# Kernel tuning notes

Measured on AMD Instinct MI355X. Metric: run time of the kernel, lower is better.

## Reference

```python
import jax, jax.numpy as jnp
import numpy as np

D = 1024
H = 16
HD = D // H


def quant_linear(x, W, b):
    # global abs-max fake quant, then linear (W is [out, in] like torch)
    scale = jnp.abs(x).max() / 127.0 + 1e-8
    xq = jnp.clip(jnp.round(x / scale), -128.0, 127.0) * scale
    return xq @ W.T + b


def rmsnorm(x, w, eps=1e-6):
    ms = jnp.mean(x * x, axis=-1, keepdims=True)
    return w * (x * jax.lax.rsqrt(ms + eps))


def setup_inputs() -> dict:
    key = jax.random.key(0)
    ks = jax.random.split(key, 20)
    def lin(k, out_f, in_f):
        bound = 1.0 / np.sqrt(in_f)
        kw, kb = jax.random.split(k)
        W = jax.random.uniform(kw, (out_f, in_f), jnp.float32, -bound, bound)
        b = jax.random.uniform(kb, (out_f,), jnp.float32, -bound, bound)
        return W, b
    x = jax.random.normal(ks[0], (4, 2048, D), jnp.float32)
    h_prev = jax.random.normal(ks[1], (4, 2048, D), jnp.float32)
    rec_W, rec_b = lin(ks[2], D, D)
    in_proj_w = jax.random.normal(ks[3], (3 * D, D), jnp.float32) * (1.0 / np.sqrt(D))
    in_proj_b = jnp.zeros((3 * D,), jnp.float32)
    out_w, out_b = lin(ks[4], D, D)
    w1_W, w1_b = lin(ks[5], 4 * D, D)
    w2_W, w2_b = lin(ks[6], 4 * D, D)
    w3_W, w3_b = lin(ks[7], D, 4 * D)
    # depthwise conv1d: torch weight [D, 1, 5]
    cb = 1.0 / np.sqrt(5)
    conv_w = jax.random.uniform(ks[8], (D, 1, 5), jnp.float32, -cb, cb)
    conv_b = jax.random.uniform(ks[9], (D,), jnp.float32, -cb, cb)
    return dict(x=x, h_prev=h_prev,
                norm1_w=jnp.ones((D,), jnp.float32), norm2_w=jnp.ones((D,), jnp.float32),
                decay=jnp.full((D,), -0.2, jnp.float32),
                rec_W=rec_W, rec_b=rec_b,
                in_proj_w=in_proj_w, in_proj_b=in_proj_b, out_w=out_w, out_b=out_b,
                conv_w=conv_w, conv_b=conv_b,
                w1_W=w1_W, w1_b=w1_b, w2_W=w2_W, w2_b=w2_b, w3_W=w3_W, w3_b=w3_b)


def reference(x, h_prev, norm1_w, norm2_w, decay, rec_W, rec_b,
              in_proj_w, in_proj_b, out_w, out_b, conv_w, conv_b,
              w1_W, w1_b, w2_W, w2_b, w3_W, w3_b):
    B, S, _ = x.shape
    nx = rmsnorm(x, norm1_w)
    # decay-gated recurrence (single step)
    h_rec = jnp.tanh(quant_linear(nx, rec_W, rec_b) + jnp.exp(decay) * h_prev)
    # multi-head self-attention (torch MultiheadAttention, batch_first)
    qkv = nx @ in_proj_w.T + in_proj_b  # [B,S,3D]
    q, k, v = jnp.split(qkv, 3, axis=-1)
    q = q.reshape(B, S, H, HD)
    k = k.reshape(B, S, H, HD)
    v = v.reshape(B, S, H, HD)
    scores = jnp.einsum('bqhd,bkhd->bhqk', q, k) / np.sqrt(HD)
    attn = jax.nn.softmax(scores, axis=-1)
    h_attn = jnp.einsum('bhqk,bkhd->bqhd', attn, v).reshape(B, S, D)
    h_attn = h_attn @ out_w.T + out_b
    # depthwise conv along sequence
    xc = jnp.swapaxes(nx, 1, 2)  # [B,D,S]
    hc = jax.lax.conv_general_dilated(xc, conv_w, window_strides=(1,), padding=[(2, 2)],
                                      feature_group_count=D,
                                      dimension_numbers=('NCH', 'OIH', 'NCH'))
    h_conv = jnp.swapaxes(hc + conv_b[None, :, None], 1, 2)
    x = x + h_rec + h_attn + h_conv
    # SwiGLU FFN with fake-quant linears
    nx2 = rmsnorm(x, norm2_w)
    ff = quant_linear(jax.nn.silu(quant_linear(nx2, w1_W, w1_b)) * quant_linear(nx2, w2_W, w2_b), w3_W, w3_b)
    x = x + ff
    return (x, h_rec)
```

## Files before the change

kernel.cpp:

```cpp
#include <hip/hip_runtime.h>
#include <stdint.h>

#define DD 1024
#define SS 2048
#define HH 16
#define HDD 64
#define NTOK 8192

typedef unsigned short u16;
typedef __attribute__((ext_vector_type(8))) short bf16x8;
typedef __attribute__((ext_vector_type(4))) float f32x4;
typedef __attribute__((ext_vector_type(4))) u16 u16x4;
typedef __attribute__((address_space(1))) unsigned int u32a1;
typedef __attribute__((address_space(3))) unsigned int u32a3;

__device__ __forceinline__ float bf2f(u16 u){
  union { float f; unsigned v; } c; c.v = ((unsigned)u) << 16; return c.f;
}
__device__ __forceinline__ u16 f2bf(float f){
  unsigned x = __float_as_uint(f);
  x = (x + 0x7fffu + ((x >> 16) & 1u)) >> 16;
  return (u16)x;
}
__device__ __forceinline__ void async16(const u16* g, u16* l){
  __builtin_amdgcn_global_load_lds((const u32a1*)g, (u32a3*)l, 16, 0, 0);
}
__device__ __forceinline__ int vswz(int row){
  return (((row & 7) ^ ((row >> 3) & 7)) << 4);
}


__global__ __launch_bounds__(256) void f32_to_bf16_kernel(
    const float* __restrict__ in, u16* __restrict__ out, int n)
{
  int i = (blockIdx.x * 256 + threadIdx.x) * 4;
  if (i >= n) return;
  float4 v = *(const float4*)(in + i);
  u16x4 o; o.x = f2bf(v.x); o.y = f2bf(v.y); o.z = f2bf(v.z); o.w = f2bf(v.w);
  *(u16x4*)(out + i) = o;
}

__global__ __launch_bounds__(256) void rmsnorm_absmax_kernel(
    const float* __restrict__ xin, const float* __restrict__ wgt,
    u16* __restrict__ nxo, float* __restrict__ pmax)
{
  const int row = blockIdx.x, t = threadIdx.x;
  const int w = t >> 6, l = t & 63;
  float4 xv = *(const float4*)(xin + (size_t)row * DD + t * 4);
  float ss = xv.x*xv.x + xv.y*xv.y + xv.z*xv.z + xv.w*xv.w;
  #pragma unroll
  for (int m = 1; m < 64; m <<= 1) ss += __shfl_xor(ss, m, 64);
  __shared__ float red[4];
  __shared__ float redm[4];
  if (l == 0) red[w] = ss;
  __syncthreads();
  float tot = red[0] + red[1] + red[2] + red[3];
  float rstd = rsqrtf(tot * (1.f / DD) + 1e-6f);
  float4 wv = *(const float4*)(wgt + t * 4);
  float o0 = xv.x * rstd * wv.x;
  float o1 = xv.y * rstd * wv.y;
  float o2 = xv.z * rstd * wv.z;
  float o3 = xv.w * rstd * wv.w;
  u16x4 ov; ov.x = f2bf(o0); ov.y = f2bf(o1); ov.z = f2bf(o2); ov.w = f2bf(o3);
  *(u16x4*)(nxo + (size_t)row * DD + t * 4) = ov;
  float lm = fmaxf(fmaxf(fabsf(o0), fabsf(o1)), fmaxf(fabsf(o2), fabsf(o3)));
  #pragma unroll
  for (int m = 1; m < 64; m <<= 1) lm = fmaxf(lm, __shfl_xor(lm, m, 64));
  if (l == 0) redm[w] = lm;
  __syncthreads();
  if (t == 0)
    pmax[row] = fmaxf(fmaxf(redm[0], redm[1]), fmaxf(redm[2], redm[3]));
}

__global__ __launch_bounds__(1024) void amax_reduce_kernel(
    const float* __restrict__ p, int n, unsigned* __restrict__ amax)
{
  const int t = threadIdx.x;
  float m = 0.f;
  for (int i = t; i < n; i += 1024) m = fmaxf(m, p[i]);
  #pragma unroll
  for (int msk = 1; msk < 64; msk <<= 1) m = fmaxf(m, __shfl_xor(m, msk, 64));
  __shared__ float red[16];
  if ((t & 63) == 0) red[t >> 6] = m;
  __syncthreads();
  if (t == 0){
    float mm = red[0];
    #pragma unroll
    for (int i = 1; i < 16; i++) mm = fmaxf(mm, red[i]);
    *amax = __float_as_uint(mm);
  }
}

__global__ __launch_bounds__(256) void quantize_kernel(
    const u16* __restrict__ in, u16* __restrict__ outq,
    const unsigned* __restrict__ amax, int n)
{
  int i = (blockIdx.x * 256 + threadIdx.x) * 8;
  if (i >= n) return;
  float am = __uint_as_float(*amax);
  float scale = am / 127.f + 1e-8f;
  float inv = 1.f / scale;
  uint4 a = *(const uint4*)(in + i);
  u16* u = (u16*)&a;
  #pragma unroll
  for (int j = 0; j < 8; j++){
    float v = bf2f(u[j]);
    float q = rintf(v * inv);
    q = fminf(127.f, fmaxf(-128.f, q));
    u[j] = f2bf(q * scale);
  }
  *(uint4*)(outq + i) = a;
}

template<int MODE>
__global__ __launch_bounds__(256) void gemm_bt(
    const u16* __restrict__ A, const u16* __restrict__ Wt,
    const float* __restrict__ bias, int M, int N, int K,
    void* __restrict__ out,
    const float* __restrict__ e0, const float* __restrict__ e1,
    const float* __restrict__ e2, const float* __restrict__ e3,
    const u16* __restrict__ eb0, float* __restrict__ pmax)
{
  __shared__ __align__(16) u16 Ash[128 * 32];
  __shared__ __align__(16) u16 Bsh[128 * 32];
  const int t = threadIdx.x, w = t >> 6, l = t & 63;
  const int brow = blockIdx.y * 128, bcol = blockIdx.x * 128;
  const int wr = w >> 1, wc = w & 1;
  f32x4 acc[4][4] = {};

  const u16* Ab = A + (size_t)brow * K;
  const u16* Bb = Wt + (size_t)bcol * K;
  const int r4 = t >> 2, c8 = (t & 3) * 8;

  for (int k0 = 0; k0 < K; k0 += 32){
    #pragma unroll
    for (int j = 0; j < 2; j++){
      async16(Ab + (size_t)(j * 64 + r4) * K + k0 + c8, &Ash[(j * 64 + r4) * 32 + c8]);
      async16(Bb + (size_t)(j * 64 + r4) * K + k0 + c8, &Bsh[(j * 64 + r4) * 32 + c8]);
    }
    __syncthreads();
    bf16x8 af[4], bfr[4];
    #pragma unroll
    for (int m = 0; m < 4; m++)
      af[m] = *(const bf16x8*)&Ash[(wr * 64 + m * 16 + (l & 15)) * 32 + (l >> 4) * 8];
    #pragma unroll
    for (int n = 0; n < 4; n++)
      bfr[n] = *(const bf16x8*)&Bsh[(wc * 64 + n * 16 + (l & 15)) * 32 + (l >> 4) * 8];
    #pragma unroll
    for (int m = 0; m < 4; m++)
      #pragma unroll
      for (int n = 0; n < 4; n++)
        acc[m][n] = __builtin_amdgcn_mfma_f32_16x16x32_bf16(af[m], bfr[n], acc[m][n], 0, 0, 0);
    __syncthreads();
  }

  float localmax = 0.f;
  #pragma unroll
  for (int m = 0; m < 4; m++){
    #pragma unroll
    for (int n = 0; n < 4; n++){
      #pragma unroll
      for (int r = 0; r < 4; r++){
        const int row = brow + wr * 64 + m * 16 + (l >> 4) * 4 + r;
        const int col = bcol + wc * 64 + n * 16 + (l & 15);
        const size_t idx = (size_t)row * N + col;
        float v = acc[m][n][r] + bias[col];
        if constexpr (MODE == 0){
          ((u16*)out)[idx] = f2bf(v);
        } else if constexpr (MODE == 1){
          v = tanhf(v + expf(e0[col]) * e1[idx]);
          ((float*)out)[idx] = v;
        } else if constexpr (MODE == 2){
          const int s = row & (SS - 1);
          float hc = e3[col];
          const u16* np = eb0 + idx;
          #pragma unroll
          for (int j = 0; j < 5; j++){
            int sn = s + j - 2;
            if (sn >= 0 && sn < SS) hc += bf2f(np[(j - 2) * DD]) * e2[col * 5 + j];
          }
          ((float*)out)[idx] = v + e0[idx] + e1[idx] + hc;
        } else if constexpr (MODE == 3){
          float h1v = bf2f(eb0[idx]);
          float g = h1v / (1.f + expf(-h1v)) * v;
          ((u16*)out)[idx] = f2bf(g);
          localmax = fmaxf(localmax, fabsf(g));
        } else {
          ((float*)out)[idx] += v;
        }
      }
    }
  }
  if constexpr (MODE == 3){
    #pragma unroll
    for (int msk = 1; msk < 64; msk <<= 1)
      localmax = fmaxf(localmax, __shfl_xor(localmax, msk, 64));
    __shared__ float wmax[4];
    if (l == 0) wmax[w] = localmax;
    __syncthreads();
    if (t == 0)
      pmax[blockIdx.y * gridDim.x + blockIdx.x] =
          fmaxf(fmaxf(wmax[0], wmax[1]), fmaxf(wmax[2], wmax[3]));
  }
}

__global__ __launch_bounds__(256) void attn_kernel(
    const u16* __restrict__ qkv, u16* __restrict__ attn_out)
{
  const int qb = blockIdx.x;
  const int bh = blockIdx.y;
  const int h = bh & (HH - 1), b = bh >> 4;
  const int t = threadIdx.x, w = t >> 6, l = t & 63;
  const int lm = l & 15, lh = l >> 4;
  const int tok0 = b * SS;
  const size_t rstr = 3 * DD;

  __shared__ __align__(16) u16 Ksh[64 * 64];
  __shared__ __align__(16) u16 Vsh[64 * 64];
  __shared__ __align__(16) u16 Psh[4][32 * 64];

  const int qr0 = qb * 128 + w * 32;
  bf16x8 qf[2][2];
  #pragma unroll
  for (int qt = 0; qt < 2; qt++){
    const u16* qp = qkv + (size_t)(tok0 + qr0 + qt * 16 + lm) * rstr + h * HDD + lh * 8;
    qf[qt][0] = *(const bf16x8*)qp;
    qf[qt][1] = *(const bf16x8*)(qp + 32);
  }
  f32x4 acc_o[2][4] = {};
  float mrun[2][4], lrun[2][4];
  #pragma unroll
  for (int qt = 0; qt < 2; qt++)
    #pragma unroll
    for (int r = 0; r < 4; r++){ mrun[qt][r] = -1e30f; lrun[qt][r] = 0.f; }

  for (int kv0 = 0; kv0 < SS; kv0 += 64){
    #pragma unroll
    for (int j = 0; j < 2; j++){
      const int krl = j * 32 + (t >> 3);
      const int c8 = (t & 7) * 8;
      const size_t rowb = (size_t)(tok0 + kv0 + krl) * rstr + h * HDD + c8;
      uint4 kv4 = *(const uint4*)(qkv + rowb + DD);
      *(uint4*)((char*)Ksh + (((krl * 64 + c8) * 2) ^ ((krl & 7) << 4))) = kv4;
      uint4 vv4 = *(const uint4*)(qkv + rowb + 2 * DD);
      const u16* vs = (const u16*)&vv4;
      #pragma unroll
      for (int i = 0; i < 8; i++){
        const int vr = c8 + i;
        *(u16*)((char*)Vsh + (((vr * 64 + krl) * 2) ^ vswz(vr))) = vs[i];
      }
    }
    __syncthreads();

    #pragma unroll
    for (int qt = 0; qt < 2; qt++){
      f32x4 sc[4];
      #pragma unroll
      for (int n = 0; n < 4; n++){
        f32x4 z = {};
        #pragma unroll
        for (int kk = 0; kk < 2; kk++){
          const int krow = n * 16 + lm;
          bf16x8 kf = *(const bf16x8*)((const char*)Ksh +
              (((krow * 64 + kk * 32 + lh * 8) * 2) ^ ((krow & 7) << 4)));
          z = __builtin_amdgcn_mfma_f32_16x16x32_bf16(qf[qt][kk], kf, z, 0, 0, 0);
        }
        sc[n] = z * 0.125f;
      }
      #pragma unroll
      for (int r = 0; r < 4; r++){
        float m0 = fmaxf(fmaxf(sc[0][r], sc[1][r]), fmaxf(sc[2][r], sc[3][r]));
        #pragma unroll
        for (int msk = 1; msk < 16; msk <<= 1) m0 = fmaxf(m0, __shfl_xor(m0, msk, 64));
        float mn = fmaxf(mrun[qt][r], m0);
        float al = __expf(mrun[qt][r] - mn);
        mrun[qt][r] = mn;
        lrun[qt][r] *= al;
        #pragma unroll
        for (int n = 0; n < 4; n++) acc_o[qt][n][r] *= al;
      }
      float rsum[4] = {0.f, 0.f, 0.f, 0.f};
      #pragma unroll
      for (int n = 0; n < 4; n++)
        #pragma unroll
        for (int r = 0; r < 4; r++){
          float p = __expf(sc[n][r] - mrun[qt][r]);
          sc[n][r] = p;
          rsum[r] += p;
        }
      #pragma unroll
      for (int r = 0; r < 4; r++){
        #pragma unroll
        for (int msk = 1; msk < 16; msk <<= 1) rsum[r] += __shfl_xor(rsum[r], msk, 64);
        lrun[qt][r] += rsum[r];
      }
      #pragma unroll
      for (int n = 0; n < 4; n++)
        #pragma unroll
        for (int r = 0; r < 4; r++){
          const int prow = qt * 16 + lh * 4 + r;
          *(u16*)((char*)&Psh[w][0] +
              (((prow * 64 + n * 16 + lm) * 2) ^ vswz(prow))) = f2bf(sc[n][r]);
        }
    }

    #pragma unroll
    for (int kk = 0; kk < 2; kk++){
      bf16x8 pf[2];
      #pragma unroll
      for (int qt = 0; qt < 2; qt++){
        const int prow = qt * 16 + lm;
        pf[qt] = *(const bf16x8*)((const char*)&Psh[w][0] +
            (((prow * 64 + kk * 32 + lh * 8) * 2) ^ vswz(prow)));
      }
      #pragma unroll
      for (int n = 0; n < 4; n++){
        const int vr = n * 16 + lm;
        bf16x8 vf = *(const bf16x8*)((const char*)Vsh +
            (((vr * 64 + kk * 32 + lh * 8) * 2) ^ vswz(vr)));
        acc_o[0][n] = __builtin_amdgcn_mfma_f32_16x16x32_bf16(pf[0], vf, acc_o[0][n], 0, 0, 0);
        acc_o[1][n] = __builtin_amdgcn_mfma_f32_16x16x32_bf16(pf[1], vf, acc_o[1][n], 0, 0, 0);
      }
    }
    __syncthreads();
  }

  #pragma unroll
  for (int qt = 0; qt < 2; qt++)
    #pragma unroll
    for (int r = 0; r < 4; r++){
      float inv = 1.f / lrun[qt][r];
      const int row = tok0 + qr0 + qt * 16 + lh * 4 + r;
      #pragma unroll
      for (int n = 0; n < 4; n++)
        attn_out[(size_t)row * DD + h * HDD + n * 16 + lm] = f2bf(acc_o[qt][n][r] * inv);
    }
}


extern "C" void kernel_launch(void* const* d_in, const int* in_sizes, int n_in,
                              void* d_out, int out_size, void* d_ws, size_t ws_size,
                              hipStream_t stream)
{
  (void)in_sizes; (void)n_in; (void)out_size; (void)ws_size;
  const float* x       = (const float*)d_in[0];
  const float* h_prev  = (const float*)d_in[1];
  const float* norm1_w = (const float*)d_in[2];
  const float* norm2_w = (const float*)d_in[3];
  const float* decay   = (const float*)d_in[4];
  const float* rec_W   = (const float*)d_in[5];
  const float* rec_b   = (const float*)d_in[6];
  const float* inp_W   = (const float*)d_in[7];
  const float* inp_b   = (const float*)d_in[8];
  const float* out_W   = (const float*)d_in[9];
  const float* out_b   = (const float*)d_in[10];
  const float* conv_w  = (const float*)d_in[11];
  const float* conv_b  = (const float*)d_in[12];
  const float* w1_W    = (const float*)d_in[13];
  const float* w1_b    = (const float*)d_in[14];
  const float* w2_W    = (const float*)d_in[15];
  const float* w2_b    = (const float*)d_in[16];
  const float* w3_W    = (const float*)d_in[17];
  const float* w3_b    = (const float*)d_in[18];

  const size_t NDe = (size_t)NTOK * DD;
  float* out_x = (float*)d_out;
  float* out_h = (float*)d_out + NDe;

  char* ws = (char*)d_ws;
  unsigned* amax1 = (unsigned*)ws;
  unsigned* amax2 = amax1 + 1;
  unsigned* amax3 = amax1 + 2;
  size_t off = 256;
  u16* Wrec = (u16*)(ws + off); off += (size_t)DD * DD * 2;
  u16* Winp = (u16*)(ws + off); off += (size_t)3 * DD * DD * 2;
  u16* Wout = (u16*)(ws + off); off += (size_t)DD * DD * 2;
  u16* W1   = (u16*)(ws + off); off += (size_t)4 * DD * DD * 2;
  u16* W2   = (u16*)(ws + off); off += (size_t)4 * DD * DD * 2;
  u16* W3   = (u16*)(ws + off); off += (size_t)4 * DD * DD * 2;
  u16* nx   = (u16*)(ws + off); off += NDe * 2;
  u16* xq   = (u16*)(ws + off); off += NDe * 2;
  u16* big  = (u16*)(ws + off); off += (size_t)NTOK * 4096 * 2;
  float* pmax1 = (float*)(ws + off); off += NTOK * 4;
  float* pmax2 = (float*)(ws + off); off += NTOK * 4;
  float* pmax3 = (float*)(ws + off); off += 2048 * 4;
  u16* qkvp    = big;
  u16* attnout = big + (size_t)NTOK * 3 * DD;

  f32_to_bf16_kernel<<<dim3(1024),  dim3(256), 0, stream>>>(rec_W, Wrec, DD * DD);
  f32_to_bf16_kernel<<<dim3(3072),  dim3(256), 0, stream>>>(inp_W, Winp, 3 * DD * DD);
  f32_to_bf16_kernel<<<dim3(1024),  dim3(256), 0, stream>>>(out_W, Wout, DD * DD);
  f32_to_bf16_kernel<<<dim3(4096),  dim3(256), 0, stream>>>(w1_W, W1, 4 * DD * DD);
  f32_to_bf16_kernel<<<dim3(4096),  dim3(256), 0, stream>>>(w2_W, W2, 4 * DD * DD);
  f32_to_bf16_kernel<<<dim3(4096),  dim3(256), 0, stream>>>(w3_W, W3, 4 * DD * DD);

  rmsnorm_absmax_kernel<<<dim3(NTOK), dim3(256), 0, stream>>>(x, norm1_w, nx, pmax1);
  amax_reduce_kernel<<<dim3(1), dim3(1024), 0, stream>>>(pmax1, NTOK, amax1);
  quantize_kernel<<<dim3(4096), dim3(256), 0, stream>>>(nx, xq, amax1, (int)NDe);

  gemm_bt<1><<<dim3(8, 64), dim3(256), 0, stream>>>(xq, Wrec, rec_b, NTOK, DD, DD,
      out_h, decay, h_prev, nullptr, nullptr, nullptr, nullptr);
  gemm_bt<0><<<dim3(24, 64), dim3(256), 0, stream>>>(nx, Winp, inp_b, NTOK, 3 * DD, DD,
      qkvp, nullptr, nullptr, nullptr, nullptr, nullptr, nullptr);
  attn_kernel<<<dim3(16, 64), dim3(256), 0, stream>>>(qkvp, attnout);
  gemm_bt<2><<<dim3(8, 64), dim3(256), 0, stream>>>(attnout, Wout, out_b, NTOK, DD, DD,
      out_x, x, out_h, conv_w, conv_b, nx, nullptr);

  rmsnorm_absmax_kernel<<<dim3(NTOK), dim3(256), 0, stream>>>(out_x, norm2_w, nx, pmax2);
  amax_reduce_kernel<<<dim3(1), dim3(1024), 0, stream>>>(pmax2, NTOK, amax2);
  quantize_kernel<<<dim3(4096), dim3(256), 0, stream>>>(nx, xq, amax2, (int)NDe);
  gemm_bt<0><<<dim3(32, 64), dim3(256), 0, stream>>>(xq, W1, w1_b, NTOK, 4 * DD, DD,
      big, nullptr, nullptr, nullptr, nullptr, nullptr, nullptr);
  gemm_bt<3><<<dim3(32, 64), dim3(256), 0, stream>>>(xq, W2, w2_b, NTOK, 4 * DD, DD,
      big, nullptr, nullptr, nullptr, nullptr, big, pmax3);
  amax_reduce_kernel<<<dim3(1), dim3(1024), 0, stream>>>(pmax3, 2048, amax3);
  quantize_kernel<<<dim3(16384), dim3(256), 0, stream>>>(big, big, amax3, NTOK * 4096);
  gemm_bt<4><<<dim3(8, 64), dim3(256), 0, stream>>>(big, W3, w3_b, NTOK, DD, 4 * DD,
      out_x, nullptr, nullptr, nullptr, nullptr, nullptr, nullptr);
}
```

Measured before the change: 1.076 ms.

## Compute transposed scores in attention and pass P via shuffles instead of LDS

Swaps the MFMA operand order so each lane holds one query row's scores. Per-row max and sum then need only two cross-lane shuffles instead of four per row, and the running max and sum shrink to one scalar per query tile. The probability tile is packed to bf16 with v_cvt_pk_bf16_f32 and redistributed with ds_bpermute-style shuffles into the A-operand layout, which removes the per-wave LDS P buffer and its scattered 2-byte stores. The cost is many more shuffle instructions in the P·V stage and broadcast shuffles when rescaling the accumulator.

```diff
diff --git a/kernel.cpp b/kernel.cpp
--- a/kernel.cpp
+++ b/kernel.cpp
@@ -27,6 +27,11 @@
 }
 __device__ __forceinline__ int vswz(int row){
   return (((row & 7) ^ ((row >> 3) & 7)) << 4);
+}
+__device__ __forceinline__ unsigned cvtpk(float lo, float hi){
+  unsigned r;
+  asm("v_cvt_pk_bf16_f32 %0, %1, %2" : "=v"(r) : "v"(lo), "v"(hi));
+  return r;
 }
 
 
@@ -217,7 +222,6 @@
 
   __shared__ __align__(16) u16 Ksh[64 * 64];
   __shared__ __align__(16) u16 Vsh[64 * 64];
-  __shared__ __align__(16) u16 Psh[4][32 * 64];
 
   const int qr0 = qb * 128 + w * 32;
   bf16x8 qf[2][2];
@@ -228,11 +232,8 @@
     qf[qt][1] = *(const bf16x8*)(qp + 32);
   }
   f32x4 acc_o[2][4] = {};
-  float mrun[2][4], lrun[2][4];
-  #pragma unroll
-  for (int qt = 0; qt < 2; qt++)
-    #pragma unroll
-    for (int r = 0; r < 4; r++){ mrun[qt][r] = -1e30f; lrun[qt][r] = 0.f; }
+  float mrun[2] = {-1e30f, -1e30f};
+  float lrun[2] = {0.f, 0.f};
 
   for (int kv0 = 0; kv0 < SS; kv0 += 64){
     #pragma unroll
@@ -252,6 +253,7 @@
     }
     __syncthreads();
 
+    unsigned pk[2][4][2];
     #pragma unroll
     for (int qt = 0; qt < 2; qt++){
       f32x4 sc[4];
@@ -263,78 +265,86 @@
           const int krow = n * 16 + lm;
           bf16x8 kf = *(const bf16x8*)((const char*)Ksh +
               (((krow * 64 + kk * 32 + lh * 8) * 2) ^ ((krow & 7) << 4)));
-          z = __builtin_amdgcn_mfma_f32_16x16x32_bf16(qf[qt][kk], kf, z, 0, 0, 0);
+          z = __builtin_amdgcn_mfma_f32_16x16x32_bf16(kf, qf[qt][kk], z, 0, 0, 0);
         }
-        sc[n] = z * 0.125f;
-      }
+        sc[n] = z;
+      }
+      float m0 = sc[0][0];
+      #pragma unroll
+      for (int n = 0; n < 4; n++)
+        #pragma unroll
+        for (int r = 0; r < 4; r++) m0 = fmaxf(m0, sc[n][r]);
+      m0 = fmaxf(m0, __shfl_xor(m0, 16, 64));
+      m0 = fmaxf(m0, __shfl_xor(m0, 32, 64));
+      m0 *= 0.125f;
+      float mn = fmaxf(mrun[qt], m0);
+      float al = __expf(mrun[qt] - mn);
+      mrun[qt] = mn;
+      lrun[qt] *= al;
       #pragma unroll
       for (int r = 0; r < 4; r++){
-        float m0 = fmaxf(fmaxf(sc[0][r], sc[1][r]), fmaxf(sc[2][r], sc[3][r]));
+        float alr = __shfl(al, lh * 4 + r, 64);
         #pragma unroll
-        for (int msk = 1; msk < 16; msk <<= 1) m0 = fmaxf(m0, __shfl_xor(m0, msk, 64));
-        float mn = fmaxf(mrun[qt][r], m0);
-        float al = __expf(mrun[qt][r] - mn);
-        mrun[qt][r] = mn;
-        lrun[qt][r] *= al;
-        #pragma unroll
-        for (int n = 0; n < 4; n++) acc_o[qt][n][r] *= al;
-      }
-      float rsum[4] = {0.f, 0.f, 0.f, 0.f};
+        for (int n = 0; n < 4; n++) acc_o[qt][n][r] *= alr;
+      }
+      float rs = 0.f;
       #pragma unroll
       for (int n = 0; n < 4; n++)
         #pragma unroll
         for (int r = 0; r < 4; r++){
-          float p = __expf(sc[n][r] - mrun[qt][r]);
+          float p = __expf(fmaf(sc[n][r], 0.125f, -mn));
           sc[n][r] = p;
-          rsum[r] += p;
+          rs += p;
         }
-      #pragma unroll
-      for (int r = 0; r < 4; r++){
+      rs += __shfl_xor(rs, 16, 64);
+      rs += __shfl_xor(rs, 32, 64);
+      lrun[qt] += rs;
+      #pragma unroll
+      for (int n = 0; n < 4; n++){
+        pk[qt][n][0] = cvtpk(sc[n][0], sc[n][1]);
+        pk[qt][n][1] = cvtpk(sc[n][2], sc[n][3]);
+      }
+    }
+
+    #pragma unroll
+    for (int kk = 0; kk < 2; kk++){
+      bf16x8 pA[2];
+      #pragma unroll
+      for (int qt = 0; qt < 2; qt++){
+        union { bf16x8 v; unsigned u[4]; } pa;
         #pragma unroll
-        for (int msk = 1; msk < 16; msk <<= 1) rsum[r] += __shfl_xor(rsum[r], msk, 64);
-        lrun[qt][r] += rsum[r];
-      }
-      #pragma unroll
-      for (int n = 0; n < 4; n++)
-        #pragma unroll
-        for (int r = 0; r < 4; r++){
-          const int prow = qt * 16 + lh * 4 + r;
-          *(u16*)((char*)&Psh[w][0] +
-              (((prow * 64 + n * 16 + lm) * 2) ^ vswz(prow))) = f2bf(sc[n][r]);
+        for (int w4 = 0; w4 < 4; w4++){
+          const int src = lm + 16 * (2 * (lh & 1) + (w4 >> 1));
+          unsigned a0 = (unsigned)__shfl((int)pk[qt][2 * kk + 0][w4 & 1], src, 64);
+          unsigned a1 = (unsigned)__shfl((int)pk[qt][2 * kk + 1][w4 & 1], src, 64);
+          pa.u[w4] = (lh >> 1) ? a1 : a0;
         }
-    }
-
-    #pragma unroll
-    for (int kk = 0; kk < 2; kk++){
-      bf16x8 pf[2];
-      #pragma unroll
-      for (int qt = 0; qt < 2; qt++){
-        const int prow = qt * 16 + lm;
-        pf[qt] = *(const bf16x8*)((const char*)&Psh[w][0] +
-            (((prow * 64 + kk * 32 + lh * 8) * 2) ^ vswz(prow)));
+        pA[qt] = pa.v;
       }
       #pragma unroll
       for (int n = 0; n < 4; n++){
         const int vr = n * 16 + lm;
         bf16x8 vf = *(const bf16x8*)((const char*)Vsh +
             (((vr * 64 + kk * 32 + lh * 8) * 2) ^ vswz(vr)));
-        acc_o[0][n] = __builtin_amdgcn_mfma_f32_16x16x32_bf16(pf[0], vf, acc_o[0][n], 0, 0, 0);
-        acc_o[1][n] = __builtin_amdgcn_mfma_f32_16x16x32_bf16(pf[1], vf, acc_o[1][n], 0, 0, 0);
+        acc_o[0][n] = __builtin_amdgcn_mfma_f32_16x16x32_bf16(pA[0], vf, acc_o[0][n], 0, 0, 0);
+        acc_o[1][n] = __builtin_amdgcn_mfma_f32_16x16x32_bf16(pA[1], vf, acc_o[1][n], 0, 0, 0);
       }
     }
     __syncthreads();
   }
 
   #pragma unroll
-  for (int qt = 0; qt < 2; qt++)
+  for (int qt = 0; qt < 2; qt++){
+    const float inv = 1.f / lrun[qt];
     #pragma unroll
     for (int r = 0; r < 4; r++){
-      float inv = 1.f / lrun[qt][r];
+      const float invr = __shfl(inv, lh * 4 + r, 64);
       const int row = tok0 + qr0 + qt * 16 + lh * 4 + r;
       #pragma unroll
       for (int n = 0; n < 4; n++)
-        attn_out[(size_t)row * DD + h * HDD + n * 16 + lm] = f2bf(acc_o[qt][n][r] * inv);
-    }
+        attn_out[(size_t)row * DD + h * HDD + n * 16 + lm] = f2bf(acc_o[qt][n][r] * invr);
+    }
+  }
 }
 
 
```

Result: no change. 1.078 ms (+0.1%).
